# Kernel optimization log

Hardware: AMD Instinct MI355X
Metric: run time of the kernel (lower is better)

## Reference

```python
import jax, jax.numpy as jnp
import numpy as np

B, T, C = 2, 2048, 1024
N_HEAD = 16
HEAD = C // N_HEAD


def setup_inputs() -> dict:
    key = jax.random.key(0)
    k1, k2, k3 = jax.random.split(key, 3)
    x = jax.random.normal(k1, (B, T, C), dtype=jnp.float32)
    w_qkv = jax.random.normal(k2, (3 * C, C), dtype=jnp.float32) * 0.02
    w_proj = jax.random.normal(k3, (C, C), dtype=jnp.float32) * 0.02
    return {"x": x, "w_qkv": w_qkv, "w_proj": w_proj}


def reference(x, w_qkv, w_proj):
    b, t, c = x.shape
    # c_attn: y = x @ W^T  (no bias). Split rows of W into q/k/v blocks.
    wq, wk, wv = jnp.split(w_qkv, 3, axis=0)            # each [C, C]
    q = (x @ wq.T).reshape(b, t, N_HEAD, HEAD)          # [B,T,H,D]
    k = (x @ wk.T).reshape(b, t, N_HEAD, HEAD)
    v = (x @ wv.T).reshape(b, t, N_HEAD, HEAD)
    scale = 1.0 / np.sqrt(HEAD).astype(np.float32)
    scores = jnp.einsum('bqhd,bkhd->bhqk', q, k) * scale  # [B,H,T,T]
    causal = jnp.tril(jnp.ones((t, t), dtype=bool))
    scores = jnp.where(causal, scores, -jnp.inf)
    attn = jax.nn.softmax(scores, axis=-1)               # [B,H,T,T]
    out = jnp.einsum('bhqk,bkhd->bqhd', attn, v).reshape(b, t, c)
    return out @ w_proj.T
```

## Files before the change

kernel.cpp:

```cpp
#include <hip/hip_runtime.h>
#include <hip/hip_bf16.h>


typedef __attribute__((ext_vector_type(8))) short bf16x8;
typedef __attribute__((ext_vector_type(4))) short bf16x4;
typedef __attribute__((ext_vector_type(4))) float floatx4;

#define MFMA16(a, b, c) __builtin_amdgcn_mfma_f32_16x16x32_bf16((a), (b), (c), 0, 0, 0)

#if __has_builtin(__builtin_amdgcn_exp2f)
#define EXP2F(x) __builtin_amdgcn_exp2f(x)
#else
#define EXP2F(x) exp2f(x)
#endif

static constexpr int Bc = 2, Tc = 2048, Cc = 1024, Hc = 16, Dc = 64;
static constexpr size_t QKV_STRIDE = (size_t)Bc * Hc * Tc * Dc;
static constexpr float KSL2E = 0.125f * 1.44269504088896f;

__device__ __forceinline__ bf16x8 load8(const __hip_bfloat16* p) {
    return *(const bf16x8*)p;
}

__device__ __forceinline__ bf16x8 load8_lds(const __hip_bfloat16* p) {
    const bf16x4 lo = *(const bf16x4*)p;
    const bf16x4 hi = *(const bf16x4*)(p + 4);
    bf16x8 r;
    r[0] = lo[0]; r[1] = lo[1]; r[2] = lo[2]; r[3] = lo[3];
    r[4] = hi[0]; r[5] = hi[1]; r[6] = hi[2]; r[7] = hi[3];
    return r;
}

__device__ __forceinline__ short f2b(float x) {
    union { __hip_bfloat16 h; short s; } u;
    u.h = __float2bfloat16(x);
    return u.s;
}

__device__ __forceinline__ bf16x8 pack8(floatx4 a, floatx4 b) {
    bf16x8 r;
    r[0] = f2b(a[0]); r[1] = f2b(a[1]); r[2] = f2b(a[2]); r[3] = f2b(a[3]);
    r[4] = f2b(b[0]); r[5] = f2b(b[1]); r[6] = f2b(b[2]); r[7] = f2b(b[3]);
    return r;
}

__device__ __forceinline__ void gl2lds16(const void* g, void* l) {
    __builtin_amdgcn_global_load_lds(
        (const __attribute__((address_space(1))) void*)g,
        (__attribute__((address_space(3))) void*)l, 16, 0, 0);
}

__global__ __launch_bounds__(256) void cvt_bf16(
    const float* __restrict__ in, __hip_bfloat16* __restrict__ out, int n8) {
    const int i = blockIdx.x * 256 + threadIdx.x;
    if (i < n8) {
        const floatx4 a = *(const floatx4*)&in[(size_t)i * 8];
        const floatx4 b = *(const floatx4*)&in[(size_t)i * 8 + 4];
        *(bf16x8*)&out[(size_t)i * 8] = pack8(a, b);
    }
}

__global__ __launch_bounds__(256) void gemm_qkv_bf16(
    const __hip_bfloat16* __restrict__ A,
    const __hip_bfloat16* __restrict__ W,
    __hip_bfloat16* __restrict__ qkv) {
    __shared__ __hip_bfloat16 As16[128 * 32];
    __shared__ __hip_bfloat16 Bs16[128 * 32];
    const int K = Cc;
    const int lane = threadIdx.x & 63;
    const int wave = threadIdx.x >> 6;
    const int waveM = wave >> 1, waveN = wave & 1;
    const int mBase = blockIdx.x * 128;
    const int nBase = blockIdx.y * 128;
    const int idx16 = lane & 15;
    const int quad = lane >> 4;
    const int aRow = lane >> 2, aPos = lane & 3;

    floatx4 acc[4][4] = {};

    for (int k0 = 0; k0 < K; k0 += 32) {
        __syncthreads();
#pragma unroll
        for (int s = 0; s < 2; s++) {
            const int r0 = wave * 32 + s * 16;
            const int row = r0 + aRow;
            const int cg = aPos ^ (row & 3);
            gl2lds16(A + (size_t)(mBase + row) * K + k0 + cg * 8, &As16[r0 * 32]);
            gl2lds16(W + (size_t)(nBase + row) * K + k0 + cg * 8, &Bs16[r0 * 32]);
        }
        __syncthreads();

        bf16x8 af[4], bfr[4];
#pragma unroll
        for (int i = 0; i < 4; i++) {
            const int rr = waveM * 64 + i * 16 + idx16;
            af[i] = *(const bf16x8*)&As16[rr * 32 + ((quad ^ (rr & 3)) * 8)];
        }
#pragma unroll
        for (int j = 0; j < 4; j++) {
            const int rr = waveN * 64 + j * 16 + idx16;
            bfr[j] = *(const bf16x8*)&Bs16[rr * 32 + ((quad ^ (rr & 3)) * 8)];
        }
#pragma unroll
        for (int i = 0; i < 4; i++)
#pragma unroll
            for (int j = 0; j < 4; j++)
                acc[i][j] = MFMA16(af[i], bfr[j], acc[i][j]);
    }

#pragma unroll
    for (int i = 0; i < 4; i++) {
#pragma unroll
        for (int j = 0; j < 4; j++) {
            const int n = nBase + waveN * 64 + j * 16 + idx16;
            const int part = n >> 10;
            const int rem = n & 1023;
            const int h = rem >> 6, d = rem & 63;
#pragma unroll
            for (int r = 0; r < 4; r++) {
                const int m = mBase + waveM * 64 + i * 16 + quad * 4 + r;
                const int bb = m >> 11, t = m & 2047;
                const size_t o = (size_t)part * QKV_STRIDE +
                                 (((size_t)(bb * Hc + h)) * Tc + t) * Dc + d;
                qkv[o] = __float2bfloat16(acc[i][j][r]);
            }
        }
    }
}

__global__ __launch_bounds__(256) void gemm_proj_bf16(
    const __hip_bfloat16* __restrict__ A,
    const __hip_bfloat16* __restrict__ W,
    float* __restrict__ out) {
    __shared__ __hip_bfloat16 As16[128 * 32];
    __shared__ __hip_bfloat16 Bs16[64 * 32];
    const int K = Cc;
    const int lane = threadIdx.x & 63;
    const int wave = threadIdx.x >> 6;
    const int waveM = wave >> 1, waveN = wave & 1;
    const int mBase = blockIdx.x * 128;
    const int nBase = blockIdx.y * 64;
    const int idx16 = lane & 15;
    const int quad = lane >> 4;
    const int aRow = lane >> 2, aPos = lane & 3;

    floatx4 acc[4][2] = {};

    for (int k0 = 0; k0 < K; k0 += 32) {
        __syncthreads();
#pragma unroll
        for (int s = 0; s < 2; s++) {
            const int r0 = wave * 32 + s * 16;
            const int row = r0 + aRow;
            const int cg = aPos ^ (row & 3);
            gl2lds16(A + (size_t)(mBase + row) * K + k0 + cg * 8, &As16[r0 * 32]);
        }
        {
            const int r0 = wave * 16;
            const int row = r0 + aRow;
            const int cg = aPos ^ (row & 3);
            gl2lds16(W + (size_t)(nBase + row) * K + k0 + cg * 8, &Bs16[r0 * 32]);
        }
        __syncthreads();

        bf16x8 af[4], bfr[2];
#pragma unroll
        for (int i = 0; i < 4; i++) {
            const int rr = waveM * 64 + i * 16 + idx16;
            af[i] = *(const bf16x8*)&As16[rr * 32 + ((quad ^ (rr & 3)) * 8)];
        }
#pragma unroll
        for (int j = 0; j < 2; j++) {
            const int rr = waveN * 32 + j * 16 + idx16;
            bfr[j] = *(const bf16x8*)&Bs16[rr * 32 + ((quad ^ (rr & 3)) * 8)];
        }
#pragma unroll
        for (int i = 0; i < 4; i++)
#pragma unroll
            for (int j = 0; j < 2; j++)
                acc[i][j] = MFMA16(af[i], bfr[j], acc[i][j]);
    }

#pragma unroll
    for (int i = 0; i < 4; i++) {
#pragma unroll
        for (int j = 0; j < 2; j++) {
            const int n = nBase + waveN * 32 + j * 16 + idx16;
#pragma unroll
            for (int r = 0; r < 4; r++) {
                const int m = mBase + waveM * 64 + i * 16 + quad * 4 + r;
                out[(size_t)m * Cc + n] = acc[i][j][r];
            }
        }
    }
}

__global__ __launch_bounds__(256) void transpose_v(
    const __hip_bfloat16* __restrict__ v,
    __hip_bfloat16* __restrict__ vt) {
    __shared__ unsigned short tile[64][65];
    const int t0 = blockIdx.x * 64;
    const int h = blockIdx.y, b = blockIdx.z;
    const size_t base = ((size_t)(b * Hc + h)) * Tc * Dc;
    const unsigned short* vp = (const unsigned short*)v + base;
    unsigned short* vtp = (unsigned short*)vt + base;

    for (int e = threadIdx.x; e < 4096; e += 256) {
        const int tl = e >> 6, d = e & 63;
        tile[tl][d] = vp[(size_t)(t0 + tl) * Dc + d];
    }
    __syncthreads();
    for (int e = threadIdx.x; e < 4096; e += 256) {
        const int d = e >> 6, tl = e & 63;
        vtp[(size_t)d * Tc + t0 + tl] = tile[tl][d];
    }
}

__global__ __launch_bounds__(512) void attn_fold(
    const __hip_bfloat16* __restrict__ qkv,
    const __hip_bfloat16* __restrict__ vt,
    __hip_bfloat16* __restrict__ aout) {
    __shared__ floatx4 smem4[6400];
    char* const smem = (char*)smem4;
    __hip_bfloat16* const kA = (__hip_bfloat16*)smem;
    __hip_bfloat16* const vA = kA + 8192;
    __hip_bfloat16* const kB = vA + 8192;
    __hip_bfloat16* const vB = kB + 8192;
    __hip_bfloat16* const Pb = vB + 8192;
    float* const comb = (float*)smem;

    const int lane = threadIdx.x & 63;
    const int wave = threadIdx.x >> 6;
    const int col = lane & 15;
    const int quad = lane >> 4;
    const int p = blockIdx.x;
    const int h = blockIdx.y;
    const int b = blockIdx.z;
    const int H = 15 - p, L = p;
    const int lightEnd = 2 * p + 2;
    const int w3 = wave & 3;

    const size_t headOff = ((size_t)(b * Hc + h)) * Tc * Dc;
    const __hip_bfloat16* qp = qkv + headOff;
    const __hip_bfloat16* kp = qkv + QKV_STRIDE + headOff;
    const __hip_bfloat16* vtp = vt + headOff;

    int qB = ((wave < 4) ? H : L) * 128 + w3 * 32;
    int qtw = (qB + 31) >> 6;
    int q0a = qB + quad * 4;
    int q0b = q0a + 16;
    bf16x8 qfa[2], qfb[2];
    {
        const int qrA = qB + col, qrB = qrA + 16;
        qfa[0] = load8(qp + (size_t)qrA * Dc + quad * 8);
        qfa[1] = load8(qp + (size_t)qrA * Dc + 32 + quad * 8);
        qfb[0] = load8(qp + (size_t)qrB * Dc + quad * 8);
        qfb[1] = load8(qp + (size_t)qrB * Dc + 32 + quad * 8);
    }

    floatx4 oa[4] = {}, ob[4] = {};
    float la[4] = {0.f, 0.f, 0.f, 0.f}, lb[4] = {0.f, 0.f, 0.f, 0.f};

    auto stageA = [&](int kt, int buf) {
        const int keyBase = kt * 64;
#pragma unroll
        for (int s = 0; s < 2; s++) {
            const int blk = w3 * 2 + s;
            const int row = blk * 8 + (lane >> 3);
            const int g = (lane & 7) ^ (row & 7);
            gl2lds16(kp + (size_t)(keyBase + row) * Dc + g * 8,
                     kA + buf * 4096 + blk * 512);
            gl2lds16(vtp + (size_t)row * Tc + keyBase + g * 8,
                     vA + buf * 4096 + blk * 512);
        }
    };
    auto stageB = [&](int kt, int buf) {
        const int keyBase = kt * 64;
#pragma unroll
        for (int s = 0; s < 2; s++) {
            const int blk = w3 * 2 + s;
            const int row = blk * 8 + (lane >> 3);
            const int g = (lane & 7) ^ (row & 7);
            gl2lds16(kp + (size_t)(keyBase + row) * Dc + g * 8,
                     kB + buf * 4096 + blk * 512);
            gl2lds16(vtp + (size_t)row * Tc + keyBase + g * 8,
                     vB + buf * 4096 + blk * 512);
        }
    };

    auto computeTile = [&](const __hip_bfloat16* kS, const __hip_bfloat16* vS,
                           int keyBase) {
        bf16x8 kc0[4], kc1[4], vc0[4], vc1[4];
#pragma unroll
        for (int j = 0; j < 4; j++) {
            const int kr = j * 16 + col;
            const int m8 = (kr & 7) * 8;
            kc0[j] = load8(&kS[kr * 64 + ((quad * 8) ^ m8)]);
            kc1[j] = load8(&kS[kr * 64 + ((32 + quad * 8) ^ m8)]);
            vc0[j] = load8(&vS[kr * 64 + ((quad * 8) ^ m8)]);
            vc1[j] = load8(&vS[kr * 64 + ((32 + quad * 8) ^ m8)]);
        }

        floatx4 sa[4], sb[4];
#pragma unroll
        for (int j = 0; j < 4; j++) {
            floatx4 a0 = {0.f, 0.f, 0.f, 0.f};
            a0 = MFMA16(qfa[0], kc0[j], a0);
            sa[j] = MFMA16(qfa[1], kc1[j], a0);
            floatx4 b0 = {0.f, 0.f, 0.f, 0.f};
            b0 = MFMA16(qfb[0], kc0[j], b0);
            sb[j] = MFMA16(qfb[1], kc1[j], b0);
        }

        __hip_bfloat16* Pw = Pb + (size_t)wave * 2304;
#pragma unroll
        for (int j = 0; j < 4; j++) {
            const int key = keyBase + j * 16 + col;
#pragma unroll
            for (int r = 0; r < 4; r++) {
                float pa = EXP2F(sa[j][r] * KSL2E);
                pa = (key > q0a + r) ? 0.f : pa;
                la[r] += pa;
                Pw[(quad * 4 + r) * 72 + j * 16 + col] = __float2bfloat16(pa);
                float pb = EXP2F(sb[j][r] * KSL2E);
                pb = (key > q0b + r) ? 0.f : pb;
                lb[r] += pb;
                Pw[1152 + (quad * 4 + r) * 72 + j * 16 + col] = __float2bfloat16(pb);
            }
        }

        const bf16x8 pa0 = load8_lds(&Pw[col * 72 + quad * 8]);
        const bf16x8 pa1 = load8_lds(&Pw[col * 72 + 32 + quad * 8]);
        const bf16x8 pb0 = load8_lds(&Pw[1152 + col * 72 + quad * 8]);
        const bf16x8 pb1 = load8_lds(&Pw[1152 + col * 72 + 32 + quad * 8]);
#pragma unroll
        for (int j = 0; j < 4; j++) {
            oa[j] = MFMA16(pa0, vc0[j], oa[j]);
            oa[j] = MFMA16(pa1, vc1[j], oa[j]);
            ob[j] = MFMA16(pb0, vc0[j], ob[j]);
            ob[j] = MFMA16(pb1, vc1[j], ob[j]);
        }
    };

    auto outStore = [&](int qB_) {
#pragma unroll
        for (int off = 1; off < 16; off <<= 1)
#pragma unroll
            for (int r = 0; r < 4; r++) {
                la[r] += __shfl_xor(la[r], off, 64);
                lb[r] += __shfl_xor(lb[r], off, 64);
            }
        const int qa = qB_ + quad * 4, qbb = qa + 16;
#pragma unroll
        for (int j = 0; j < 4; j++) {
            const int d = j * 16 + col;
#pragma unroll
            for (int r = 0; r < 4; r++) {
                aout[((size_t)(b * Tc + qa + r)) * Cc + h * 64 + d] =
                    __float2bfloat16(oa[j][r] / la[r]);
                aout[((size_t)(b * Tc + qbb + r)) * Cc + h * 64 + d] =
                    __float2bfloat16(ob[j][r] / lb[r]);
            }
        }
    };

    if (wave < 4) stageA(0, 0);

    for (int i = 0; i < 17; i++) {
        __syncthreads();
        if (i < 16) {
            if (wave < 4) stageA(i + 1, (i + 1) & 1);
            else if (i + 1 >= lightEnd) stageB(i + 16 - 2 * p, (i + 1) & 1);
        }
        if (wave >= 4 && i == lightEnd) {
            outStore(qB);
#pragma unroll
            for (int j = 0; j < 4; j++) {
                oa[j] = floatx4{0.f, 0.f, 0.f, 0.f};
                ob[j] = floatx4{0.f, 0.f, 0.f, 0.f};
            }
#pragma unroll
            for (int r = 0; r < 4; r++) { la[r] = 0.f; lb[r] = 0.f; }
            qB = H * 128 + w3 * 32;
            qtw = (qB + 31) >> 6;
            q0a = qB + quad * 4;
            q0b = q0a + 16;
            const int qrA = qB + col, qrB2 = qrA + 16;
            qfa[0] = load8(qp + (size_t)qrA * Dc + quad * 8);
            qfa[1] = load8(qp + (size_t)qrA * Dc + 32 + quad * 8);
            qfb[0] = load8(qp + (size_t)qrB2 * Dc + quad * 8);
            qfb[1] = load8(qp + (size_t)qrB2 * Dc + 32 + quad * 8);
        }
        if (wave < 4) {
            computeTile(kA + (i & 1) * 4096, vA + (i & 1) * 4096, i * 64);
        } else if (i < lightEnd) {
            if (i <= qtw)
                computeTile(kA + (i & 1) * 4096, vA + (i & 1) * 4096, i * 64);
        } else {
            const int kt = i + 15 - 2 * p;
            if (kt <= qtw)
                computeTile(kB + (i & 1) * 4096, vB + (i & 1) * 4096, kt * 64);
        }
        __syncthreads();
    }

    if (wave >= 4) {
        float* c = comb + (size_t)(wave - 4) * 2560;
#pragma unroll
        for (int j = 0; j < 4; j++)
#pragma unroll
            for (int r = 0; r < 4; r++) {
                c[(j * 4 + r) * 64 + lane] = oa[j][r];
                c[(16 + j * 4 + r) * 64 + lane] = ob[j][r];
            }
#pragma unroll
        for (int r = 0; r < 4; r++) {
            c[(32 + r) * 64 + lane] = la[r];
            c[(36 + r) * 64 + lane] = lb[r];
        }
    }
    __syncthreads();
    if (wave < 4) {
        float* c = comb + (size_t)wave * 2560;
#pragma unroll
        for (int j = 0; j < 4; j++)
#pragma unroll
            for (int r = 0; r < 4; r++) {
                oa[j][r] += c[(j * 4 + r) * 64 + lane];
                ob[j][r] += c[(16 + j * 4 + r) * 64 + lane];
            }
#pragma unroll
        for (int r = 0; r < 4; r++) {
            la[r] += c[(32 + r) * 64 + lane];
            lb[r] += c[(36 + r) * 64 + lane];
        }
        outStore(qB);
    }
}

__global__ __launch_bounds__(256) void gemm_qkv(
    const float* __restrict__ A,
    const float* __restrict__ W,
    __hip_bfloat16* __restrict__ qkv) {
    __shared__ float As[128 * 32];
    __shared__ float Bs[128 * 32];
    const int K = Cc;
    const int lane = threadIdx.x & 63;
    const int wave = threadIdx.x >> 6;
    const int waveM = wave >> 1, waveN = wave & 1;
    const int mBase = blockIdx.x * 128;
    const int nBase = blockIdx.y * 128;
    const int idx16 = lane & 15;
    const int quad = lane >> 4;
    const int ldRow = lane >> 3;
    const int ldPos = lane & 7;

    floatx4 acc[4][4] = {};

    for (int k0 = 0; k0 < K; k0 += 32) {
        __syncthreads();
#pragma unroll
        for (int s = 0; s < 4; s++) {
            const int r0 = wave * 32 + s * 8;
            const int row = r0 + ldRow;
            const int cg = ldPos ^ (row & 7);
            gl2lds16(A + (size_t)(mBase + row) * K + k0 + cg * 4, &As[r0 * 32]);
            gl2lds16(W + (size_t)(nBase + row) * K + k0 + cg * 4, &Bs[r0 * 32]);
        }
        __syncthreads();

        bf16x8 af[4], bfr[4];
#pragma unroll
        for (int i = 0; i < 4; i++) {
            const int rr = waveM * 64 + i * 16 + idx16;
            const floatx4 a0 = *(const floatx4*)&As[rr * 32 + (((quad * 2) ^ (rr & 7)) * 4)];
            const floatx4 a1 = *(const floatx4*)&As[rr * 32 + (((quad * 2 + 1) ^ (rr & 7)) * 4)];
            af[i] = pack8(a0, a1);
        }
#pragma unroll
        for (int j = 0; j < 4; j++) {
            const int rr = waveN * 64 + j * 16 + idx16;
            const floatx4 b0 = *(const floatx4*)&Bs[rr * 32 + (((quad * 2) ^ (rr & 7)) * 4)];
            const floatx4 b1 = *(const floatx4*)&Bs[rr * 32 + (((quad * 2 + 1) ^ (rr & 7)) * 4)];
            bfr[j] = pack8(b0, b1);
        }
#pragma unroll
        for (int i = 0; i < 4; i++)
#pragma unroll
            for (int j = 0; j < 4; j++)
                acc[i][j] = MFMA16(af[i], bfr[j], acc[i][j]);
    }

#pragma unroll
    for (int i = 0; i < 4; i++) {
#pragma unroll
        for (int j = 0; j < 4; j++) {
            const int n = nBase + waveN * 64 + j * 16 + idx16;
            const int part = n >> 10;
            const int rem = n & 1023;
            const int h = rem >> 6, d = rem & 63;
#pragma unroll
            for (int r = 0; r < 4; r++) {
                const int m = mBase + waveM * 64 + i * 16 + quad * 4 + r;
                const int bb = m >> 11, t = m & 2047;
                const size_t o = (size_t)part * QKV_STRIDE +
                                 (((size_t)(bb * Hc + h)) * Tc + t) * Dc + d;
                qkv[o] = __float2bfloat16(acc[i][j][r]);
            }
        }
    }
}

__global__ __launch_bounds__(256) void gemm_proj(
    const __hip_bfloat16* __restrict__ A,
    const float* __restrict__ W,
    float* __restrict__ out) {
    __shared__ __hip_bfloat16 As16[128 * 32];
    __shared__ float Ws[64 * 32];
    const int K = Cc;
    const int lane = threadIdx.x & 63;
    const int wave = threadIdx.x >> 6;
    const int waveM = wave >> 1, waveN = wave & 1;
    const int mBase = blockIdx.x * 128;
    const int nBase = blockIdx.y * 64;
    const int idx16 = lane & 15;
    const int quad = lane >> 4;
    const int aRow = lane >> 2, aPos = lane & 3;
    const int wRow = lane >> 3, wPos = lane & 7;

    floatx4 acc[4][2] = {};

    for (int k0 = 0; k0 < K; k0 += 32) {
        __syncthreads();
#pragma unroll
        for (int s = 0; s < 2; s++) {
            {
                const int r0 = wave * 32 + s * 16;
                const int row = r0 + aRow;
                const int cg = aPos ^ (row & 3);
                gl2lds16(A + (size_t)(mBase + row) * K + k0 + cg * 8, &As16[r0 * 32]);
            }
            {
                const int r0 = wave * 16 + s * 8;
                const int row = r0 + wRow;
                const int cg = wPos ^ (row & 7);
                gl2lds16(W + (size_t)(nBase + row) * K + k0 + cg * 4, &Ws[r0 * 32]);
            }
        }
        __syncthreads();

        bf16x8 af[4], bfr[2];
#pragma unroll
        for (int i = 0; i < 4; i++) {
            const int rr = waveM * 64 + i * 16 + idx16;
            af[i] = *(const bf16x8*)&As16[rr * 32 + ((quad ^ (rr & 3)) * 8)];
        }
#pragma unroll
        for (int j = 0; j < 2; j++) {
            const int rr = waveN * 32 + j * 16 + idx16;
            const floatx4 b0 = *(const floatx4*)&Ws[rr * 32 + (((quad * 2) ^ (rr & 7)) * 4)];
            const floatx4 b1 = *(const floatx4*)&Ws[rr * 32 + (((quad * 2 + 1) ^ (rr & 7)) * 4)];
            bfr[j] = pack8(b0, b1);
        }
#pragma unroll
        for (int i = 0; i < 4; i++)
#pragma unroll
            for (int j = 0; j < 2; j++)
                acc[i][j] = MFMA16(af[i], bfr[j], acc[i][j]);
    }

#pragma unroll
    for (int i = 0; i < 4; i++) {
#pragma unroll
        for (int j = 0; j < 2; j++) {
            const int n = nBase + waveN * 32 + j * 16 + idx16;
#pragma unroll
            for (int r = 0; r < 4; r++) {
                const int m = mBase + waveM * 64 + i * 16 + quad * 4 + r;
                out[(size_t)m * Cc + n] = acc[i][j][r];
            }
        }
    }
}

extern "C" void kernel_launch(void* const* d_in, const int* in_sizes, int n_in,
                              void* d_out, int out_size, void* d_ws, size_t ws_size,
                              hipStream_t stream) {
    const float* x = nullptr;
    const float* w_qkv = nullptr;
    const float* w_proj = nullptr;
    for (int i = 0; i < n_in; i++) {
        if (in_sizes[i] == 4194304) x = (const float*)d_in[i];
        else if (in_sizes[i] == 3145728) w_qkv = (const float*)d_in[i];
        else if (in_sizes[i] == 1048576) w_proj = (const float*)d_in[i];
    }
    float* out = (float*)d_out;

    __hip_bfloat16* qkv = (__hip_bfloat16*)d_ws;
    __hip_bfloat16* vbuf = qkv + 2 * QKV_STRIDE;
    __hip_bfloat16* vt = qkv + 3 * QKV_STRIDE;
    __hip_bfloat16* ao = vbuf;

    const size_t CVT_OFF = 8 * QKV_STRIDE;
    const size_t NEED = CVT_OFF + (4194304 + 3145728) * sizeof(__hip_bfloat16);

    if (ws_size >= NEED) {
        __hip_bfloat16* xb = (__hip_bfloat16*)((char*)d_ws + CVT_OFF);
        __hip_bfloat16* wbq = xb + 4194304;
        __hip_bfloat16* wbp = qkv;

        cvt_bf16<<<dim3(4194304 / 8 / 256), 256, 0, stream>>>(x, xb, 4194304 / 8);
        cvt_bf16<<<dim3(3145728 / 8 / 256), 256, 0, stream>>>(w_qkv, wbq, 3145728 / 8);
        gemm_qkv_bf16<<<dim3(4096 / 128, 3072 / 128), 256, 0, stream>>>(xb, wbq, qkv);
        transpose_v<<<dim3(Tc / 64, Hc, Bc), 256, 0, stream>>>(vbuf, vt);
        attn_fold<<<dim3(8, Hc, Bc), 512, 0, stream>>>(qkv, vt, ao);
        cvt_bf16<<<dim3(1048576 / 8 / 256), 256, 0, stream>>>(w_proj, wbp, 1048576 / 8);
        gemm_proj_bf16<<<dim3(4096 / 128, 1024 / 64), 256, 0, stream>>>(ao, wbp, out);
    } else {
        gemm_qkv<<<dim3(4096 / 128, 3072 / 128), 256, 0, stream>>>(x, w_qkv, qkv);
        transpose_v<<<dim3(Tc / 64, Hc, Bc), 256, 0, stream>>>(vbuf, vt);
        attn_fold<<<dim3(8, Hc, Bc), 512, 0, stream>>>(qkv, vt, ao);
        gemm_proj<<<dim3(4096 / 128, 1024 / 64), 256, 0, stream>>>(ao, w_proj, out);
    }
}
```

Baseline: 183.7 us.

## Switch attention to 32x32 MFMA and keep P in registers via lane shuffles

The attention kernel moves from 16x16x32 to 32x32x16 bf16 MFMA tiles and computes S^T = K·Q^T, so the probability matrix can be repacked into the A-operand layout with cross-half-wave shuffles. This removes the per-wave LDS round trip for P and shrinks shared memory. It also skips 32-key sub-blocks that lie entirely above the causal diagonal. The cost is larger accumulator register footprints and extra shuffle and select instructions.

After: 184.2 us. Within noise of the previous version (+0.3%).

```diff
diff --git a/kernel.cpp b/kernel.cpp
--- a/kernel.cpp
+++ b/kernel.cpp
@@ -5,8 +5,10 @@
 typedef __attribute__((ext_vector_type(8))) short bf16x8;
 typedef __attribute__((ext_vector_type(4))) short bf16x4;
 typedef __attribute__((ext_vector_type(4))) float floatx4;
+typedef __attribute__((ext_vector_type(16))) float f32x16;
 
 #define MFMA16(a, b, c) __builtin_amdgcn_mfma_f32_16x16x32_bf16((a), (b), (c), 0, 0, 0)
+#define MFMA32(a, b, c) __builtin_amdgcn_mfma_f32_32x32x16_bf16((a), (b), (c), 0, 0, 0)
 
 #if __has_builtin(__builtin_amdgcn_exp2f)
 #define EXP2F(x) __builtin_amdgcn_exp2f(x)
@@ -22,15 +24,6 @@
     return *(const bf16x8*)p;
 }
 
-__device__ __forceinline__ bf16x8 load8_lds(const __hip_bfloat16* p) {
-    const bf16x4 lo = *(const bf16x4*)p;
-    const bf16x4 hi = *(const bf16x4*)(p + 4);
-    bf16x8 r;
-    r[0] = lo[0]; r[1] = lo[1]; r[2] = lo[2]; r[3] = lo[3];
-    r[4] = hi[0]; r[5] = hi[1]; r[6] = hi[2]; r[7] = hi[3];
-    return r;
-}
-
 __device__ __forceinline__ short f2b(float x) {
     union { __hip_bfloat16 h; short s; } u;
     u.h = __float2bfloat16(x);
@@ -42,6 +35,17 @@
     r[0] = f2b(a[0]); r[1] = f2b(a[1]); r[2] = f2b(a[2]); r[3] = f2b(a[3]);
     r[4] = f2b(b[0]); r[5] = f2b(b[1]); r[6] = f2b(b[2]); r[7] = f2b(b[3]);
     return r;
+}
+
+__device__ __forceinline__ unsigned pk2(float a, float b) {
+    return (unsigned)(unsigned short)f2b(a) |
+           ((unsigned)(unsigned short)f2b(b) << 16);
+}
+
+__device__ __forceinline__ bf16x8 mk8(unsigned a, unsigned b, unsigned c, unsigned d) {
+    union { unsigned u[4]; bf16x8 v; } x;
+    x.u[0] = a; x.u[1] = b; x.u[2] = c; x.u[3] = d;
+    return x.v;
 }
 
 __device__ __forceinline__ void gl2lds16(const void* g, void* l) {
@@ -220,19 +224,18 @@
     const __hip_bfloat16* __restrict__ qkv,
     const __hip_bfloat16* __restrict__ vt,
     __hip_bfloat16* __restrict__ aout) {
-    __shared__ floatx4 smem4[6400];
+    __shared__ floatx4 smem4[4096];
     char* const smem = (char*)smem4;
     __hip_bfloat16* const kA = (__hip_bfloat16*)smem;
     __hip_bfloat16* const vA = kA + 8192;
     __hip_bfloat16* const kB = vA + 8192;
     __hip_bfloat16* const vB = kB + 8192;
-    __hip_bfloat16* const Pb = vB + 8192;
     float* const comb = (float*)smem;
 
     const int lane = threadIdx.x & 63;
     const int wave = threadIdx.x >> 6;
-    const int col = lane & 15;
-    const int quad = lane >> 4;
+    const int c31 = lane & 31;
+    const int hw = lane >> 5;
     const int p = blockIdx.x;
     const int h = blockIdx.y;
     const int b = blockIdx.z;
@@ -247,19 +250,21 @@
 
     int qB = ((wave < 4) ? H : L) * 128 + w3 * 32;
     int qtw = (qB + 31) >> 6;
-    int q0a = qB + quad * 4;
-    int q0b = q0a + 16;
-    bf16x8 qfa[2], qfb[2];
-    {
-        const int qrA = qB + col, qrB = qrA + 16;
-        qfa[0] = load8(qp + (size_t)qrA * Dc + quad * 8);
-        qfa[1] = load8(qp + (size_t)qrA * Dc + 32 + quad * 8);
-        qfb[0] = load8(qp + (size_t)qrB * Dc + quad * 8);
-        qfb[1] = load8(qp + (size_t)qrB * Dc + 32 + quad * 8);
-    }
-
-    floatx4 oa[4] = {}, ob[4] = {};
-    float la[4] = {0.f, 0.f, 0.f, 0.f}, lb[4] = {0.f, 0.f, 0.f, 0.f};
+    int qMax = qB + 31;
+    int qg = qB + c31;
+
+    bf16x8 qf0, qf1, qf2, qf3;
+    auto loadQ = [&]() {
+        const __hip_bfloat16* qr = qp + (size_t)qg * Dc + hw * 8;
+        qf0 = load8(qr);
+        qf1 = load8(qr + 16);
+        qf2 = load8(qr + 32);
+        qf3 = load8(qr + 48);
+    };
+    loadQ();
+
+    f32x16 O0 = {}, O1 = {};
+    float lacc = 0.f;
 
     auto stageA = [&](int kt, int buf) {
         const int keyBase = kt * 64;
@@ -290,77 +295,76 @@
 
     auto computeTile = [&](const __hip_bfloat16* kS, const __hip_bfloat16* vS,
                            int keyBase) {
-        bf16x8 kc0[4], kc1[4], vc0[4], vc1[4];
-#pragma unroll
-        for (int j = 0; j < 4; j++) {
-            const int kr = j * 16 + col;
-            const int m8 = (kr & 7) * 8;
-            kc0[j] = load8(&kS[kr * 64 + ((quad * 8) ^ m8)]);
-            kc1[j] = load8(&kS[kr * 64 + ((32 + quad * 8) ^ m8)]);
-            vc0[j] = load8(&vS[kr * 64 + ((quad * 8) ^ m8)]);
-            vc1[j] = load8(&vS[kr * 64 + ((32 + quad * 8) ^ m8)]);
-        }
-
-        floatx4 sa[4], sb[4];
-#pragma unroll
-        for (int j = 0; j < 4; j++) {
-            floatx4 a0 = {0.f, 0.f, 0.f, 0.f};
-            a0 = MFMA16(qfa[0], kc0[j], a0);
-            sa[j] = MFMA16(qfa[1], kc1[j], a0);
-            floatx4 b0 = {0.f, 0.f, 0.f, 0.f};
-            b0 = MFMA16(qfb[0], kc0[j], b0);
-            sb[j] = MFMA16(qfb[1], kc1[j], b0);
-        }
-
-        __hip_bfloat16* Pw = Pb + (size_t)wave * 2304;
-#pragma unroll
-        for (int j = 0; j < 4; j++) {
-            const int key = keyBase + j * 16 + col;
-#pragma unroll
-            for (int r = 0; r < 4; r++) {
-                float pa = EXP2F(sa[j][r] * KSL2E);
-                pa = (key > q0a + r) ? 0.f : pa;
-                la[r] += pa;
-                Pw[(quad * 4 + r) * 72 + j * 16 + col] = __float2bfloat16(pa);
-                float pb = EXP2F(sb[j][r] * KSL2E);
-                pb = (key > q0b + r) ? 0.f : pb;
-                lb[r] += pb;
-                Pw[1152 + (quad * 4 + r) * 72 + j * 16 + col] = __float2bfloat16(pb);
+#pragma unroll
+        for (int kb = 0; kb < 2; kb++) {
+            if (keyBase + kb * 32 <= qMax) {
+                const int kr = kb * 32 + c31;
+                const int m8 = kr & 7;
+                f32x16 S = {};
+                S = MFMA32(load8(&kS[kr * 64 + (((0 + hw) ^ m8) * 8)]), qf0, S);
+                S = MFMA32(load8(&kS[kr * 64 + (((2 + hw) ^ m8) * 8)]), qf1, S);
+                S = MFMA32(load8(&kS[kr * 64 + (((4 + hw) ^ m8) * 8)]), qf2, S);
+                S = MFMA32(load8(&kS[kr * 64 + (((6 + hw) ^ m8) * 8)]), qf3, S);
+
+                unsigned w[8];
+#pragma unroll
+                for (int r = 0; r < 16; r += 2) {
+                    const int key0 = keyBase + kb * 32 +
+                                     (r & 3) + 8 * (r >> 2) + 4 * hw;
+                    float p0 = EXP2F(S[r] * KSL2E);
+                    p0 = (key0 > qg) ? 0.f : p0;
+                    float p1 = EXP2F(S[r + 1] * KSL2E);
+                    p1 = (key0 + 1 > qg) ? 0.f : p1;
+                    lacc += p0 + p1;
+                    w[r >> 1] = pk2(p0, p1);
+                }
+
+                const unsigned s0 = (unsigned)__shfl_xor((int)w[0], 32, 64);
+                const unsigned s1 = (unsigned)__shfl_xor((int)w[1], 32, 64);
+                const unsigned s2 = (unsigned)__shfl_xor((int)w[2], 32, 64);
+                const unsigned s3 = (unsigned)__shfl_xor((int)w[3], 32, 64);
+                const unsigned s4 = (unsigned)__shfl_xor((int)w[4], 32, 64);
+                const unsigned s5 = (unsigned)__shfl_xor((int)w[5], 32, 64);
+                const unsigned s6 = (unsigned)__shfl_xor((int)w[6], 32, 64);
+                const unsigned s7 = (unsigned)__shfl_xor((int)w[7], 32, 64);
+                const bf16x8 pA0 = mk8(hw ? s2 : w[0],
+                                       hw ? s3 : w[1],
+                                       hw ? w[2] : s0,
+                                       hw ? w[3] : s1);
+                const bf16x8 pA1 = mk8(hw ? s6 : w[4],
+                                       hw ? s7 : w[5],
+                                       hw ? w[6] : s4,
+                                       hw ? w[7] : s5);
+
+                {
+                    const int vr = c31;
+                    const int vm = vr & 7;
+                    const bf16x8 vf0 = load8(&vS[vr * 64 + (((kb * 4 + hw) ^ vm) * 8)]);
+                    const bf16x8 vf1 = load8(&vS[vr * 64 + (((kb * 4 + 2 + hw) ^ vm) * 8)]);
+                    O0 = MFMA32(pA0, vf0, O0);
+                    O0 = MFMA32(pA1, vf1, O0);
+                }
+                {
+                    const int vr = 32 + c31;
+                    const int vm = vr & 7;
+                    const bf16x8 vf0 = load8(&vS[vr * 64 + (((kb * 4 + hw) ^ vm) * 8)]);
+                    const bf16x8 vf1 = load8(&vS[vr * 64 + (((kb * 4 + 2 + hw) ^ vm) * 8)]);
+                    O1 = MFMA32(pA0, vf0, O1);
+                    O1 = MFMA32(pA1, vf1, O1);
+                }
             }
         }
-
-        const bf16x8 pa0 = load8_lds(&Pw[col * 72 + quad * 8]);
-        const bf16x8 pa1 = load8_lds(&Pw[col * 72 + 32 + quad * 8]);
-        const bf16x8 pb0 = load8_lds(&Pw[1152 + col * 72 + quad * 8]);
-        const bf16x8 pb1 = load8_lds(&Pw[1152 + col * 72 + 32 + quad * 8]);
-#pragma unroll
-        for (int j = 0; j < 4; j++) {
-            oa[j] = MFMA16(pa0, vc0[j], oa[j]);
-            oa[j] = MFMA16(pa1, vc1[j], oa[j]);
-            ob[j] = MFMA16(pb0, vc0[j], ob[j]);
-            ob[j] = MFMA16(pb1, vc1[j], ob[j]);
-        }
     };
 
-    auto outStore = [&](int qB_) {
-#pragma unroll
-        for (int off = 1; off < 16; off <<= 1)
-#pragma unroll
-            for (int r = 0; r < 4; r++) {
-                la[r] += __shfl_xor(la[r], off, 64);
-                lb[r] += __shfl_xor(lb[r], off, 64);
-            }
-        const int qa = qB_ + quad * 4, qbb = qa + 16;
-#pragma unroll
-        for (int j = 0; j < 4; j++) {
-            const int d = j * 16 + col;
-#pragma unroll
-            for (int r = 0; r < 4; r++) {
-                aout[((size_t)(b * Tc + qa + r)) * Cc + h * 64 + d] =
-                    __float2bfloat16(oa[j][r] / la[r]);
-                aout[((size_t)(b * Tc + qbb + r)) * Cc + h * 64 + d] =
-                    __float2bfloat16(ob[j][r] / lb[r]);
-            }
+    auto outStore = [&](int qB_, float ltot) {
+#pragma unroll
+        for (int r = 0; r < 16; r++) {
+            const int qrl = (r & 3) + 8 * (r >> 2) + 4 * hw;
+            const float lr = __shfl(ltot, qrl, 64);
+            const float inv = 1.0f / lr;
+            const size_t rowOff = ((size_t)(b * Tc + qB_ + qrl)) * Cc + h * 64;
+            aout[rowOff + c31] = __float2bfloat16(O0[r] * inv);
+            aout[rowOff + 32 + c31] = __float2bfloat16(O1[r] * inv);
         }
     };
 
@@ -373,23 +377,15 @@
             else if (i + 1 >= lightEnd) stageB(i + 16 - 2 * p, (i + 1) & 1);
         }
         if (wave >= 4 && i == lightEnd) {
-            outStore(qB);
-#pragma unroll
-            for (int j = 0; j < 4; j++) {
-                oa[j] = floatx4{0.f, 0.f, 0.f, 0.f};
-                ob[j] = floatx4{0.f, 0.f, 0.f, 0.f};
-            }
-#pragma unroll
-            for (int r = 0; r < 4; r++) { la[r] = 0.f; lb[r] = 0.f; }
+            outStore(qB, lacc + __shfl_xor(lacc, 32, 64));
+#pragma unroll
+            for (int r = 0; r < 16; r++) { O0[r] = 0.f; O1[r] = 0.f; }
+            lacc = 0.f;
             qB = H * 128 + w3 * 32;
             qtw = (qB + 31) >> 6;
-            q0a = qB + quad * 4;
-            q0b = q0a + 16;
-            const int qrA = qB + col, qrB2 = qrA + 16;
-            qfa[0] = load8(qp + (size_t)qrA * Dc + quad * 8);
-            qfa[1] = load8(qp + (size_t)qrA * Dc + 32 + quad * 8);
-            qfb[0] = load8(qp + (size_t)qrB2 * Dc + quad * 8);
-            qfb[1] = load8(qp + (size_t)qrB2 * Dc + 32 + quad * 8);
+            qMax = qB + 31;
+            qg = qB + c31;
+            loadQ();
         }
         if (wave < 4) {
             computeTile(kA + (i & 1) * 4096, vA + (i & 1) * 4096, i * 64);
@@ -404,37 +400,25 @@
         __syncthreads();
     }
 
+    const float ltotOwn = lacc + __shfl_xor(lacc, 32, 64);
     if (wave >= 4) {
-        float* c = comb + (size_t)(wave - 4) * 2560;
-#pragma unroll
-        for (int j = 0; j < 4; j++)
-#pragma unroll
-            for (int r = 0; r < 4; r++) {
-                c[(j * 4 + r) * 64 + lane] = oa[j][r];
-                c[(16 + j * 4 + r) * 64 + lane] = ob[j][r];
-            }
-#pragma unroll
-        for (int r = 0; r < 4; r++) {
-            c[(32 + r) * 64 + lane] = la[r];
-            c[(36 + r) * 64 + lane] = lb[r];
-        }
+        float* c = comb + (size_t)(wave - 4) * 2112;
+#pragma unroll
+        for (int r = 0; r < 16; r++) {
+            c[r * 64 + lane] = O0[r];
+            c[(16 + r) * 64 + lane] = O1[r];
+        }
+        c[2048 + lane] = ltotOwn;
     }
     __syncthreads();
     if (wave < 4) {
-        float* c = comb + (size_t)wave * 2560;
-#pragma unroll
-        for (int j = 0; j < 4; j++)
-#pragma unroll
-            for (int r = 0; r < 4; r++) {
-                oa[j][r] += c[(j * 4 + r) * 64 + lane];
-                ob[j][r] += c[(16 + j * 4 + r) * 64 + lane];
-            }
-#pragma unroll
-        for (int r = 0; r < 4; r++) {
-            la[r] += c[(32 + r) * 64 + lane];
-            lb[r] += c[(36 + r) * 64 + lane];
-        }
-        outStore(qB);
+        float* c = comb + (size_t)wave * 2112;
+#pragma unroll
+        for (int r = 0; r < 16; r++) {
+            O0[r] += c[r * 64 + lane];
+            O1[r] += c[(16 + r) * 64 + lane];
+        }
+        outStore(qB, ltotOwn + c[2048 + lane]);
     }
 }
 
```
